# Kernel tuning notes

Hardware: AMD Instinct MI355X
Metric: run time of the kernel (lower is better)

The kernel has to match this reference:

```python
import jax, jax.numpy as jnp
import numpy as np

B, S, D_MODEL, D_ATT = 4, 4096, 512, 64
EPS = 1e-5


def setup_inputs() -> dict:
    key = jax.random.key(0)
    ks = jax.random.split(key, 10)
    s_in = 1.0 / np.sqrt(D_MODEL)
    return {
        "x": jax.random.normal(ks[0], (B, S, D_MODEL), jnp.float32),
        "Wq": jax.random.uniform(ks[1], (D_MODEL, D_ATT), jnp.float32, -s_in, s_in),
        "bq": jax.random.uniform(ks[2], (D_ATT,), jnp.float32, -s_in, s_in),
        "Wk": jax.random.uniform(ks[3], (D_MODEL, D_ATT), jnp.float32, -s_in, s_in),
        "bk": jax.random.uniform(ks[4], (D_ATT,), jnp.float32, -s_in, s_in),
        "Wv": jax.random.uniform(ks[5], (D_MODEL, D_MODEL), jnp.float32, -s_in, s_in),
        "bv": jax.random.uniform(ks[6], (D_MODEL,), jnp.float32, -s_in, s_in),
        "gamma": jnp.ones((D_MODEL,), jnp.float32),
        "beta": jnp.zeros((D_MODEL,), jnp.float32),
    }


def reference(x, Wq, bq, Wk, bk, Wv, bv, gamma, beta):
    # Linear projections (torch Linear: x @ W^T + b; here W stored as [in, out])
    q = jnp.einsum("bsd,de->bse", x, Wq) + bq          # [B,S,d_att]
    k = jnp.einsum("bsd,de->bse", x, Wk) + bk          # [B,S,d_att]
    v = jnp.einsum("bsd,de->bse", x, Wv) + bv          # [B,S,d_model]
    # NOTE: original has NO 1/sqrt(d) scaling -- faithful to source.
    scores = jnp.einsum("bqe,bke->bqk", q, k)          # [B,S,S]
    seq = x.shape[1]
    causal = jnp.tril(jnp.ones((seq, seq), dtype=bool))
    scores = jnp.where(causal, scores, -jnp.inf)
    attn = jax.nn.softmax(scores, axis=-1)
    o = jnp.einsum("bqk,bkd->bqd", attn, v)            # [B,S,d_model]
    # residual + LayerNorm over last dim
    y = x + o
    mu = jnp.mean(y, axis=-1, keepdims=True)
    var = jnp.mean(jnp.square(y - mu), axis=-1, keepdims=True)
    return (y - mu) * jax.lax.rsqrt(var + EPS) * gamma + beta
```

## Files before the change

### kernel.cpp

```cpp
#include <hip/hip_runtime.h>

#define NB 4
#define SEQ 4096
#define DM 512
#define DA 64
#define LOG2E 1.44269504f

typedef __attribute__((ext_vector_type(8))) short bf16x8;
typedef __attribute__((ext_vector_type(4))) float f32x4;
typedef __attribute__((ext_vector_type(16))) float f32x16;
typedef __attribute__((address_space(3))) unsigned int lds_u32;
typedef const __attribute__((address_space(1))) unsigned int glb_u32;

__device__ __forceinline__ unsigned short f2bf(float f) {
  unsigned u = __float_as_uint(f);
  u += 0x7fffu + ((u >> 16) & 1u);
  return (unsigned short)(u >> 16);
}

__device__ __forceinline__ float bf2f(unsigned short h) {
  return __uint_as_float(((unsigned)h) << 16);
}

__device__ __forceinline__ unsigned cvt_pk_bf16(float lo, float hi) {
  unsigned r;
  asm("v_cvt_pk_bf16_f32 %0, %1, %2" : "=v"(r) : "v"(lo), "v"(hi));
  return r;
}

__device__ __forceinline__ float fexp2(float x) {
  float r;
  asm("v_exp_f32 %0, %1" : "=v"(r) : "v"(x));
  return r;
}

__device__ __forceinline__ void g2lds16(const unsigned short* g, unsigned short* l) {
  __builtin_amdgcn_global_load_lds((glb_u32*)g, (lds_u32*)l, 16, 0, 0);
}

__global__ void prep_kernel(const float* __restrict__ x, unsigned short* __restrict__ xb,
                            const float* __restrict__ Wq, const float* __restrict__ bq,
                            const float* __restrict__ Wk, const float* __restrict__ bk,
                            const float* __restrict__ Wv, const float* __restrict__ bv,
                            unsigned short* __restrict__ Wt, float* __restrict__ bias) {
  int bid = blockIdx.x;
  if (bid < 8192) {
    size_t i = ((size_t)bid * blockDim.x + threadIdx.x) * 4;
    float4 v = *(const float4*)(x + i);
    ushort4 o;
    o.x = f2bf(v.x); o.y = f2bf(v.y); o.z = f2bf(v.z); o.w = f2bf(v.w);
    *(ushort4*)(xb + i) = o;
  } else {
    int n = bid - 8192;
    for (int k = threadIdx.x; k < DM; k += blockDim.x) {
      float w;
      if (n < 64)       w = Wq[(size_t)k * DA + n];
      else if (n < 128) w = Wk[(size_t)k * DA + (n - 64)];
      else              w = Wv[(size_t)k * DM + (n - 128)];
      Wt[(size_t)n * DM + k] = f2bf(w);
    }
    if (threadIdx.x == 0)
      bias[n] = (n < 64) ? bq[n] : (n < 128) ? bk[n - 64] : bv[n - 128];
  }
}

__launch_bounds__(256)
__global__ void proj_kernel(const unsigned short* __restrict__ xb,
                            const unsigned short* __restrict__ Wt,
                            const float* __restrict__ bias,
                            unsigned short* __restrict__ qws,
                            unsigned short* __restrict__ kp,
                            unsigned short* __restrict__ vp) {
  int C0 = blockIdx.x * 128;
  int R0 = blockIdx.y * 128;
  int tid = threadIdx.x;
  int w = tid >> 6, lane = tid & 63;
  int g = (lane >> 4) & 3, c15 = lane & 15;
  int wr = w >> 1, wc = w & 1;

  __shared__ unsigned short smem[18432];
  unsigned short* Ab = smem;
  unsigned short* Bb = smem + 8192;

  int row0 = tid >> 3;
  int scol = (tid & 7) ^ (row0 & 7);
  const unsigned short* srcA = xb + (size_t)(R0 + row0) * DM + scol * 8;
  const unsigned short* srcB = Wt + (size_t)(C0 + row0) * DM + scol * 8;

  auto stage = [&](int kk) {
    for (int r = 0; r < 4; r++)
      g2lds16(srcA + (size_t)(r * 32) * DM + kk, &Ab[(r * 32 + w * 8) * 64]);
    for (int r = 0; r < 4; r++)
      g2lds16(srcB + (size_t)(r * 32) * DM + kk, &Bb[(r * 32 + w * 8) * 64]);
  };

  f32x4 acc[4][4];
#pragma unroll
  for (int i = 0; i < 4; i++)
#pragma unroll
    for (int j = 0; j < 4; j++) acc[i][j] = (f32x4)0.0f;

  stage(0);
  for (int s = 0; s < 8; s++) {
    __syncthreads();
#pragma unroll
    for (int kc = 0; kc < 2; kc++) {
      bf16x8 a[4], bb2[4];
#pragma unroll
      for (int i = 0; i < 4; i++) {
        int row = wr * 64 + i * 16 + c15;
        a[i] = *(const bf16x8*)&Ab[row * 64 + (((kc << 2) | g) ^ (row & 7)) * 8];
      }
#pragma unroll
      for (int j = 0; j < 4; j++) {
        int row = wc * 64 + j * 16 + c15;
        bb2[j] = *(const bf16x8*)&Bb[row * 64 + (((kc << 2) | g) ^ (row & 7)) * 8];
      }
#pragma unroll
      for (int i = 0; i < 4; i++)
#pragma unroll
        for (int j = 0; j < 4; j++)
          acc[i][j] = __builtin_amdgcn_mfma_f32_16x16x32_bf16(a[i], bb2[j], acc[i][j], 0, 0, 0);
    }
    if (s < 7) {
      __syncthreads();
      stage((s + 1) * 64);
    }
  }
  __syncthreads();

  unsigned short* tw = smem + w * 4608;
  int n0 = C0 + wc * 64;
#pragma unroll
  for (int j = 0; j < 4; j++) {
    int ncol = n0 + j * 16 + c15;
    float bv_ = bias[ncol];
    float qs = (ncol < 64) ? LOG2E : 1.0f;
#pragma unroll
    for (int i = 0; i < 4; i++)
#pragma unroll
      for (int r = 0; r < 4; r++) {
        int sl = i * 16 + g * 4 + r;
        tw[sl * 72 + j * 16 + c15] = f2bf((acc[i][j][r] + bv_) * qs);
      }
  }

  int RR = R0 + wr * 64;
  int b = RR >> 12, ktc = (RR & (SEQ - 1)) >> 6;
  if (n0 == 0) {
    for (int it = 0; it < 8; it++) {
      int rid = it * 64 + lane;
      int sl = rid >> 3, grp = rid & 7;
      bf16x8 vd = *(const bf16x8*)&tw[sl * 72 + grp * 8];
      *(bf16x8*)(qws + (size_t)(RR + sl) * DA + grp * 8) = vd;
    }
  } else if (n0 == 64) {
    for (int slot = 0; slot < 8; slot++) {
      bf16x8 vd = *(const bf16x8*)&tw[lane * 72 + slot * 8];
      *(bf16x8*)(kp + ((((size_t)b * 64 + ktc) * 8 + slot) * 64 + lane) * 8) = vd;
    }
  } else {
    int dvbase = n0 - 128;
    int dv = dvbase + lane;
    int dvc2 = dv >> 7, dvrow = dv & 127;
    for (int slot = 0; slot < 8; slot++) {
      union { unsigned short u[8]; bf16x8 h8; } pk;
#pragma unroll
      for (int j = 0; j < 8; j++) {
        int key = ((slot >> 2) << 5) | (((slot >> 1) & 1) << 4) | ((j >> 2) << 3) |
                  ((slot & 1) << 2) | (j & 3);
        pk.u[j] = tw[key * 72 + lane];
      }
      *(bf16x8*)(vp + (((((size_t)(b * 4 + dvc2)) * 64 + ktc) * 8 + slot) * 128 + dvrow) * 8) = pk.h8;
    }
  }
}

__launch_bounds__(256, 3)
__global__ void attn_kernel(const unsigned short* __restrict__ qws,
                            const unsigned short* __restrict__ kp,
                            const unsigned short* __restrict__ vp,
                            unsigned short* __restrict__ ob16) {
  int x = blockIdx.x, b = x >> 2, dvc = x & 3;
  int strip = 127 - blockIdx.y;
  int qrow32 = strip * 32;
  int n = (strip >> 1) + 1;
  int tid = threadIdx.x, w = tid >> 6, lane = tid & 63;
  int l31 = lane & 31, lh = lane >> 5;

  __shared__ unsigned short abuf[4][32][138];
  __shared__ float lbuf[4][32], Lfin[32];

  size_t bS = (size_t)b * SEQ;

  bf16x8 qf[4];
#pragma unroll
  for (int c = 0; c < 4; c++)
    qf[c] = *(const bf16x8*)(qws + (bS + qrow32 + l31) * DA + c * 16 + lh * 8);

  const unsigned short* kbase = kp + (size_t)b * 64 * 4096 + lh * 512 + l31 * 8;
  const unsigned short* vbase = vp + (size_t)(b * 4 + dvc) * 64 * 8192 + lh * 1024 + l31 * 8;

  f32x16 acc[4];
#pragma unroll
  for (int dt = 0; dt < 4; dt++) acc[dt] = (f32x16)0.0f;
  float la0 = 0.0f, la1 = 0.0f, la2 = 0.0f, la3 = 0.0f;

  for (int t = w; t < n; t += 4) {
    const unsigned short* kt_ = kbase + (size_t)t * 4096;
    const unsigned short* vt_ = vbase + (size_t)t * 8192;

    bf16x8 kf[4][2];
#pragma unroll
    for (int c = 0; c < 4; c++)
#pragma unroll
      for (int s2 = 0; s2 < 2; s2++)
        kf[c][s2] = *(const bf16x8*)(kt_ + c * 1024 + s2 * 256);
    bf16x8 vbA[4];
#pragma unroll
    for (int dt = 0; dt < 4; dt++)
      vbA[dt] = *(const bf16x8*)(vt_ + dt * 256);

    f32x16 sc[2];
    sc[0] = (f32x16)0.0f; sc[1] = (f32x16)0.0f;
    __builtin_amdgcn_s_setprio(1);
#pragma unroll
    for (int c = 0; c < 4; c++)
#pragma unroll
      for (int s2 = 0; s2 < 2; s2++)
        sc[s2] = __builtin_amdgcn_mfma_f32_32x32x16_bf16(kf[c][s2], qf[c], sc[s2], 0, 0, 0);
    __builtin_amdgcn_s_setprio(0);

    if (t == n - 1) {
      int kt = t * 64, qrow = qrow32 + l31;
#pragma unroll
      for (int s2 = 0; s2 < 2; s2++)
#pragma unroll
        for (int p = 0; p < 16; p++) {
          int key = kt + s2 * 32 + (p & 3) + 8 * (p >> 2) + 4 * lh;
          if (key > qrow) sc[s2][p] = -1e30f;
        }
    }

#pragma unroll
    for (int s2 = 0; s2 < 2; s2++)
#pragma unroll
      for (int p = 0; p < 16; p += 4) {
        float p0 = fexp2(sc[s2][p + 0]);
        float p1 = fexp2(sc[s2][p + 1]);
        float p2 = fexp2(sc[s2][p + 2]);
        float p3 = fexp2(sc[s2][p + 3]);
        sc[s2][p + 0] = p0; sc[s2][p + 1] = p1;
        sc[s2][p + 2] = p2; sc[s2][p + 3] = p3;
        la0 += p0; la1 += p1; la2 += p2; la3 += p3;
      }

    bf16x8 pa[4];
#pragma unroll
    for (int c = 0; c < 4; c++) {
      union { unsigned u[4]; bf16x8 h; } pu;
      int s2 = c >> 1, o = (c & 1) * 8;
      pu.u[0] = cvt_pk_bf16(sc[s2][o + 0], sc[s2][o + 1]);
      pu.u[1] = cvt_pk_bf16(sc[s2][o + 2], sc[s2][o + 3]);
      pu.u[2] = cvt_pk_bf16(sc[s2][o + 4], sc[s2][o + 5]);
      pu.u[3] = cvt_pk_bf16(sc[s2][o + 6], sc[s2][o + 7]);
      pa[c] = pu.h;
    }

    __builtin_amdgcn_s_setprio(1);
#pragma unroll
    for (int c = 0; c < 4; c++) {
      bf16x8 vbB[4];
      if (c < 3) {
#pragma unroll
        for (int dt = 0; dt < 4; dt++)
          vbB[dt] = *(const bf16x8*)(vt_ + (c + 1) * 2048 + dt * 256);
      }
#pragma unroll
      for (int dt = 0; dt < 4; dt++)
        acc[dt] = __builtin_amdgcn_mfma_f32_32x32x16_bf16(vbA[dt], pa[c], acc[dt], 0, 0, 0);
      if (c < 3) {
#pragma unroll
        for (int dt = 0; dt < 4; dt++) vbA[dt] = vbB[dt];
      }
    }
    __builtin_amdgcn_s_setprio(0);
  }

  float l_run = (la0 + la1) + (la2 + la3);
  l_run += __shfl_xor(l_run, 32);
  if (lh == 0) lbuf[w][l31] = l_run;
  __syncthreads();
  if (w == 0 && lh == 0)
    Lfin[l31] = lbuf[0][l31] + lbuf[1][l31] + lbuf[2][l31] + lbuf[3][l31];
#pragma unroll
  for (int dt = 0; dt < 4; dt++)
#pragma unroll
    for (int p = 0; p < 16; p += 2) {
      int dv = dt * 32 + (p & 3) + 8 * (p >> 2) + 4 * lh;
      *(unsigned*)&abuf[w][l31][dv] = cvt_pk_bf16(acc[dt][p], acc[dt][p + 1]);
    }
  __syncthreads();

  int q = w * 8 + (l31 >> 2);
  int ch = (l31 & 3) * 32 + lh * 16;
  float s[16];
#pragma unroll
  for (int k = 0; k < 16; k++) s[k] = 0.0f;
#pragma unroll
  for (int v = 0; v < 4; v++) {
    bf16x8 a0 = *(const bf16x8*)&abuf[v][q][ch];
    bf16x8 a1 = *(const bf16x8*)&abuf[v][q][ch + 8];
#pragma unroll
    for (int k = 0; k < 8; k++) {
      s[k] += bf2f((unsigned short)a0[k]);
      s[8 + k] += bf2f((unsigned short)a1[k]);
    }
  }
  float inv = 1.0f / Lfin[q];
  union { unsigned u[8]; bf16x8 h[2]; } o;
#pragma unroll
  for (int k = 0; k < 8; k++)
    o.u[k] = cvt_pk_bf16(s[2 * k] * inv, s[2 * k + 1] * inv);
  unsigned short* dst = ob16 + (bS + qrow32 + q) * DM + dvc * 128 + ch;
  *(bf16x8*)dst = o.h[0];
  *(bf16x8*)(dst + 8) = o.h[1];
}

__launch_bounds__(256)
__global__ void ln_kernel(const unsigned short* __restrict__ xb,
                          const unsigned short* __restrict__ o,
                          const float* __restrict__ gamma, const float* __restrict__ beta,
                          float* __restrict__ out) {
  int wid = threadIdx.x >> 6, lane = threadIdx.x & 63;
  size_t row = (size_t)blockIdx.x * 4 + wid;
  size_t base = row * DM + lane * 8;
  bf16x8 xv = *(const bf16x8*)(xb + base);
  bf16x8 ov = *(const bf16x8*)(o + base);
  float y[8];
#pragma unroll
  for (int j = 0; j < 8; j++)
    y[j] = bf2f((unsigned short)xv[j]) + bf2f((unsigned short)ov[j]);
  float s1 = 0.0f, s2 = 0.0f;
  for (int j = 0; j < 8; j++) { s1 += y[j]; s2 += y[j] * y[j]; }
  for (int m = 1; m < 64; m <<= 1) { s1 += __shfl_xor(s1, m); s2 += __shfl_xor(s2, m); }
  float mu = s1 * (1.0f / DM);
  float var = s2 * (1.0f / DM) - mu * mu;
  float rs = rsqrtf(var + 1e-5f);
  int c = lane * 8;
  for (int j = 0; j < 8; j++)
    out[base + j] = (y[j] - mu) * rs * gamma[c + j] + beta[c + j];
}

extern "C" void kernel_launch(void* const* d_in, const int* in_sizes, int n_in,
                              void* d_out, int out_size, void* d_ws, size_t ws_size,
                              hipStream_t stream) {
  const float* x     = (const float*)d_in[0];
  const float* Wq    = (const float*)d_in[1];
  const float* bq    = (const float*)d_in[2];
  const float* Wk    = (const float*)d_in[3];
  const float* bk    = (const float*)d_in[4];
  const float* Wv    = (const float*)d_in[5];
  const float* bv    = (const float*)d_in[6];
  const float* gamma = (const float*)d_in[7];
  const float* beta  = (const float*)d_in[8];
  float* out = (float*)d_out;

  char* ws = (char*)d_ws;
  unsigned short* xb   = (unsigned short*)(ws + 0);
  unsigned short* qws  = (unsigned short*)(ws + 16777216);
  unsigned short* kp   = (unsigned short*)(ws + 18874368);
  unsigned short* vp   = (unsigned short*)(ws + 20971520);
  unsigned short* ob16 = (unsigned short*)(ws + 37748736);
  unsigned short* Wt   = (unsigned short*)(ws + 54525952);
  float*          bias = (float*)(ws + 55181312);

  prep_kernel<<<8832, 256, 0, stream>>>(x, xb, Wq, bq, Wk, bk, Wv, bv, Wt, bias);
  proj_kernel<<<dim3(5, 128), 256, 0, stream>>>(xb, Wt, bias, qws, kp, vp);
  attn_kernel<<<dim3(16, 128), 256, 0, stream>>>(qws, kp, vp, ob16);
  ln_kernel<<<4096, 256, 0, stream>>>(xb, ob16, gamma, beta, out);
}
```

Before: 123.1 us.

## Fuse LayerNorm into attention and split value columns across waves

```diff
diff --git a/kernel.cpp b/kernel.cpp
--- a/kernel.cpp
+++ b/kernel.cpp
@@ -177,19 +177,22 @@
 }
 
 __launch_bounds__(256, 3)
-__global__ void attn_kernel(const unsigned short* __restrict__ qws,
-                            const unsigned short* __restrict__ kp,
-                            const unsigned short* __restrict__ vp,
-                            unsigned short* __restrict__ ob16) {
-  int x = blockIdx.x, b = x >> 2, dvc = x & 3;
-  int strip = 127 - blockIdx.y;
+__global__ void attn_ln_kernel(const unsigned short* __restrict__ qws,
+                               const unsigned short* __restrict__ kp,
+                               const unsigned short* __restrict__ vp,
+                               const unsigned short* __restrict__ xb,
+                               const float* __restrict__ gamma,
+                               const float* __restrict__ beta,
+                               float* __restrict__ out) {
+  int b = blockIdx.x;
+  int yy = blockIdx.y;
+  int strip = (yy < 64) ? yy : 191 - yy;
   int qrow32 = strip * 32;
   int n = (strip >> 1) + 1;
   int tid = threadIdx.x, w = tid >> 6, lane = tid & 63;
   int l31 = lane & 31, lh = lane >> 5;
 
-  __shared__ unsigned short abuf[4][32][138];
-  __shared__ float lbuf[4][32], Lfin[32];
+  __shared__ unsigned short obuf[32 * 516];
 
   size_t bS = (size_t)b * SEQ;
 
@@ -199,14 +202,15 @@
     qf[c] = *(const bf16x8*)(qws + (bS + qrow32 + l31) * DA + c * 16 + lh * 8);
 
   const unsigned short* kbase = kp + (size_t)b * 64 * 4096 + lh * 512 + l31 * 8;
-  const unsigned short* vbase = vp + (size_t)(b * 4 + dvc) * 64 * 8192 + lh * 1024 + l31 * 8;
+  const unsigned short* vbase = vp + (size_t)(b * 4 + w) * 64 * 8192 + lh * 1024 + l31 * 8;
 
   f32x16 acc[4];
 #pragma unroll
   for (int dt = 0; dt < 4; dt++) acc[dt] = (f32x16)0.0f;
   float la0 = 0.0f, la1 = 0.0f, la2 = 0.0f, la3 = 0.0f;
 
-  for (int t = w; t < n; t += 4) {
+  for (int t = 0; t < n; t++) {
+    __builtin_amdgcn_s_barrier();
     const unsigned short* kt_ = kbase + (size_t)t * 4096;
     const unsigned short* vt_ = vbase + (size_t)t * 8192;
 
@@ -289,67 +293,52 @@
 
   float l_run = (la0 + la1) + (la2 + la3);
   l_run += __shfl_xor(l_run, 32);
-  if (lh == 0) lbuf[w][l31] = l_run;
+  float inv = 1.0f / l_run;
+
+  unsigned* ob32 = (unsigned*)obuf;
+#pragma unroll
+  for (int dt = 0; dt < 4; dt++)
+#pragma unroll
+    for (int p = 0; p < 16; p += 2) {
+      int dvl = dt * 32 + (p & 3) + 8 * (p >> 2) + 4 * lh;
+      ob32[l31 * 258 + w * 64 + (dvl >> 1)] =
+          cvt_pk_bf16(acc[dt][p] * inv, acc[dt][p + 1] * inv);
+    }
   __syncthreads();
-  if (w == 0 && lh == 0)
-    Lfin[l31] = lbuf[0][l31] + lbuf[1][l31] + lbuf[2][l31] + lbuf[3][l31];
-#pragma unroll
-  for (int dt = 0; dt < 4; dt++)
-#pragma unroll
-    for (int p = 0; p < 16; p += 2) {
-      int dv = dt * 32 + (p & 3) + 8 * (p >> 2) + 4 * lh;
-      *(unsigned*)&abuf[w][l31][dv] = cvt_pk_bf16(acc[dt][p], acc[dt][p + 1]);
-    }
-  __syncthreads();
-
-  int q = w * 8 + (l31 >> 2);
-  int ch = (l31 & 3) * 32 + lh * 16;
-  float s[16];
-#pragma unroll
-  for (int k = 0; k < 16; k++) s[k] = 0.0f;
-#pragma unroll
-  for (int v = 0; v < 4; v++) {
-    bf16x8 a0 = *(const bf16x8*)&abuf[v][q][ch];
-    bf16x8 a1 = *(const bf16x8*)&abuf[v][q][ch + 8];
-#pragma unroll
-    for (int k = 0; k < 8; k++) {
-      s[k] += bf2f((unsigned short)a0[k]);
-      s[8 + k] += bf2f((unsigned short)a1[k]);
-    }
-  }
-  float inv = 1.0f / Lfin[q];
-  union { unsigned u[8]; bf16x8 h[2]; } o;
-#pragma unroll
-  for (int k = 0; k < 8; k++)
-    o.u[k] = cvt_pk_bf16(s[2 * k] * inv, s[2 * k + 1] * inv);
-  unsigned short* dst = ob16 + (bS + qrow32 + q) * DM + dvc * 128 + ch;
-  *(bf16x8*)dst = o.h[0];
-  *(bf16x8*)(dst + 8) = o.h[1];
-}
-
-__launch_bounds__(256)
-__global__ void ln_kernel(const unsigned short* __restrict__ xb,
-                          const unsigned short* __restrict__ o,
-                          const float* __restrict__ gamma, const float* __restrict__ beta,
-                          float* __restrict__ out) {
-  int wid = threadIdx.x >> 6, lane = threadIdx.x & 63;
-  size_t row = (size_t)blockIdx.x * 4 + wid;
-  size_t base = row * DM + lane * 8;
-  bf16x8 xv = *(const bf16x8*)(xb + base);
-  bf16x8 ov = *(const bf16x8*)(o + base);
-  float y[8];
-#pragma unroll
-  for (int j = 0; j < 8; j++)
-    y[j] = bf2f((unsigned short)xv[j]) + bf2f((unsigned short)ov[j]);
-  float s1 = 0.0f, s2 = 0.0f;
-  for (int j = 0; j < 8; j++) { s1 += y[j]; s2 += y[j] * y[j]; }
-  for (int m = 1; m < 64; m <<= 1) { s1 += __shfl_xor(s1, m); s2 += __shfl_xor(s2, m); }
-  float mu = s1 * (1.0f / DM);
-  float var = s2 * (1.0f / DM) - mu * mu;
-  float rs = rsqrtf(var + 1e-5f);
-  int c = lane * 8;
-  for (int j = 0; j < 8; j++)
-    out[base + j] = (y[j] - mu) * rs * gamma[c + j] + beta[c + j];
+
+  float4 gv0 = *(const float4*)(gamma + lane * 8);
+  float4 gv1 = *(const float4*)(gamma + lane * 8 + 4);
+  float4 bv0 = *(const float4*)(beta + lane * 8);
+  float4 bv1 = *(const float4*)(beta + lane * 8 + 4);
+#pragma unroll
+  for (int r = 0; r < 8; r++) {
+    int row = w * 8 + r;
+    bf16x8 o8 = *(const bf16x8*)&obuf[row * 516 + lane * 8];
+    bf16x8 x8 = *(const bf16x8*)(xb + (bS + qrow32 + row) * DM + lane * 8);
+    float y[8];
+#pragma unroll
+    for (int j = 0; j < 8; j++)
+      y[j] = bf2f((unsigned short)x8[j]) + bf2f((unsigned short)o8[j]);
+    float s1 = 0.0f, s2 = 0.0f;
+#pragma unroll
+    for (int j = 0; j < 8; j++) { s1 += y[j]; s2 += y[j] * y[j]; }
+    for (int m = 1; m < 64; m <<= 1) { s1 += __shfl_xor(s1, m); s2 += __shfl_xor(s2, m); }
+    float mu = s1 * (1.0f / DM);
+    float var = s2 * (1.0f / DM) - mu * mu;
+    float rs = rsqrtf(var + 1e-5f);
+    float4 o0, o1;
+    o0.x = (y[0] - mu) * rs * gv0.x + bv0.x;
+    o0.y = (y[1] - mu) * rs * gv0.y + bv0.y;
+    o0.z = (y[2] - mu) * rs * gv0.z + bv0.z;
+    o0.w = (y[3] - mu) * rs * gv0.w + bv0.w;
+    o1.x = (y[4] - mu) * rs * gv1.x + bv1.x;
+    o1.y = (y[5] - mu) * rs * gv1.y + bv1.y;
+    o1.z = (y[6] - mu) * rs * gv1.z + bv1.z;
+    o1.w = (y[7] - mu) * rs * gv1.w + bv1.w;
+    float* dst = out + (bS + qrow32 + row) * DM + lane * 8;
+    *(float4*)dst = o0;
+    *(float4*)(dst + 4) = o1;
+  }
 }
 
 extern "C" void kernel_launch(void* const* d_in, const int* in_sizes, int n_in,
@@ -371,12 +360,10 @@
   unsigned short* qws  = (unsigned short*)(ws + 16777216);
   unsigned short* kp   = (unsigned short*)(ws + 18874368);
   unsigned short* vp   = (unsigned short*)(ws + 20971520);
-  unsigned short* ob16 = (unsigned short*)(ws + 37748736);
-  unsigned short* Wt   = (unsigned short*)(ws + 54525952);
-  float*          bias = (float*)(ws + 55181312);
+  unsigned short* Wt   = (unsigned short*)(ws + 37748736);
+  float*          bias = (float*)(ws + 38404096);
 
   prep_kernel<<<8832, 256, 0, stream>>>(x, xb, Wq, bq, Wk, bk, Wv, bv, Wt, bias);
   proj_kernel<<<dim3(5, 128), 256, 0, stream>>>(xb, Wt, bias, qws, kp, vp);
-  attn_kernel<<<dim3(16, 128), 256, 0, stream>>>(qws, kp, vp, ob16);
-  ln_kernel<<<4096, 256, 0, stream>>>(xb, ob16, gamma, beta, out);
-}
+  attn_ln_kernel<<<dim3(4, 128), 256, 0, stream>>>(qws, kp, vp, xb, gamma, beta, out);
+}
```

Result: slower. 176.3 us (+43.2%).
